# Performance work log

Measured on AMD Instinct MI355X. Metric: run time of the kernel, lower is better.

The kernel has to match this reference:

```python
import jax, jax.numpy as jnp
import numpy as np

M, K, N = 32, 8192, 8192  # tokens, in_features, out_features
PACK = 8  # int4 nibbles per int32


def setup_inputs() -> dict:
    key = jax.random.key(0)
    k1, k2, k3, k4 = jax.random.split(key, 4)
    x = (jax.random.normal(k1, (M, K), dtype=jnp.float32)).astype(jnp.float16)
    # packed int4 weights: 8 signed nibbles per int32, [N, K//8]
    b_packed = jax.random.randint(k2, (N, K // PACK), 0, 2147483647, dtype=jnp.int32)
    # rowwise fp16 scales (meta), one per output row; small positive values
    scales = (jax.random.uniform(k3, (N,), dtype=jnp.float32) * 0.01 + 1e-4).astype(jnp.float16)
    bias = (jax.random.normal(k4, (N,), dtype=jnp.float32) * 0.01).astype(jnp.float16)
    return {"x": x, "b_packed": b_packed, "scales": scales, "bias": bias}


def _unpack_int4(b_packed):
    # b_packed: [N, K//8] int32 -> signed int4 values in [-8, 7], shape [N, K]
    shifts = (jnp.arange(PACK, dtype=jnp.int32) * 4)  # [8]
    nib = (b_packed[:, :, None] >> shifts) & 0xF       # [N, K//8, 8]
    q = jnp.where(nib >= 8, nib - 16, nib)             # two's-complement nibble
    return q.reshape(b_packed.shape[0], -1)            # [N, K]


def reference(x, b_packed, scales, bias):
    # Rowwise dequant: W[n, k] = q[n, k] * scale[n]  (fp16), then y = x @ W^T + bias
    q = _unpack_int4(b_packed).astype(jnp.float16)          # [N, K]
    W = q * scales[:, None]                                  # [N, K] fp16
    y = jnp.einsum('mk,nk->mn', x, W,
                   preferred_element_type=jnp.float32).astype(jnp.float16)
    y = y + bias.astype(y.dtype)
    return y
```

## Files before the change

kernel.cpp:

```cpp
#include <hip/hip_runtime.h>
#include <cstdint>

#define M_DIM 32
#define K_DIM 8192
#define N_DIM 8192

typedef _Float16 f16x8 __attribute__((ext_vector_type(8)));
typedef _Float16 f16x2 __attribute__((ext_vector_type(2)));
typedef float    f32x4 __attribute__((ext_vector_type(4)));

__device__ __forceinline__ uint32_t u4e(uint4 v, int t) {
  return (t == 0) ? v.x : (t == 1) ? v.y : (t == 2) ? v.z : v.w;
}

__device__ __forceinline__ f16x8 dq8(uint32_t w) {
  union { uint32_t u[4]; f16x8 v; } r;
  const uint32_t MASK  = 0x000F000Fu;
  const uint32_t MAGIC = 0x64086408u;
  const f16x2 magic = __builtin_bit_cast(f16x2, MAGIC);
#pragma unroll
  for (int s = 0; s < 4; ++s) {
    uint32_t t = ((w >> (4 * s)) & MASK) ^ MAGIC;
    f16x2 h = __builtin_bit_cast(f16x2, t) - magic;
    r.u[s] = __builtin_bit_cast(uint32_t, h);
  }
  return r.v;
}

__global__ __launch_bounds__(256) void xprep_kernel(
    const float* __restrict__ x, uint4* __restrict__ xp) {
  const int T = blockIdx.x * 256 + threadIdx.x;
  const int m = T >> 10;
  const int g = T & 1023;
  const f32x4* p = (const f32x4*)(x + (size_t)m * K_DIM + (size_t)g * 8);
  f32x4 lo = p[0], hi = p[1];
  union { uint4 q; f16x8 v; } o;
#pragma unroll
  for (int s = 0; s < 4; ++s) {
    o.v[2 * s]     = (_Float16)lo[s];
    o.v[2 * s + 1] = (_Float16)hi[s];
  }
  xp[(size_t)g * 32 + m] = o.q;
}

__global__ __launch_bounds__(1024, 4) void qgemm_xp(
    const uint32_t* __restrict__ bq,
    const uint4*    __restrict__ xp,
    const float*    __restrict__ sc,
    const float*    __restrict__ bi,
    float*          __restrict__ out) {
  __shared__ float red[16][32][33];

  const int tid  = threadIdx.x;
  const int w    = tid >> 6;
  const int lane = tid & 63;
  const int l16  = lane & 15;
  const int quad = lane >> 4;
  const int n0   = blockIdx.x << 5;

  const uint4* bq4 = (const uint4*)bq;
  const uint4* bp0 = bq4 + (size_t)(n0 + l16) * 256 + (w << 4) + quad;
  const uint4* bp1 = bp0 + (size_t)16 * 256;
  const uint4* ap  = xp + (size_t)(((w << 6) + (quad << 2)) * 32 + l16);

  uint4 b0[4], b1[4];
#pragma unroll
  for (int c = 0; c < 4; ++c) { b0[c] = bp0[c * 4]; b1[c] = bp1[c * 4]; }

  f32x4 acc00 = {0.f, 0.f, 0.f, 0.f};
  f32x4 acc01 = {0.f, 0.f, 0.f, 0.f};
  f32x4 acc10 = {0.f, 0.f, 0.f, 0.f};
  f32x4 acc11 = {0.f, 0.f, 0.f, 0.f};

  uint4 a0c = ap[0], a1c = ap[16];
#pragma unroll
  for (int g = 0; g < 16; ++g) {
    const int gn  = (g + 1) & 15;
    const int off = (((gn >> 2) * 16) + (gn & 3)) * 32;
    uint4 a0n = ap[off];
    uint4 a1n = ap[off + 16];

    const int c = g >> 2, t = g & 3;
    f16x8 fb0 = dq8(u4e(b0[c], t));
    f16x8 fb1 = dq8(u4e(b1[c], t));
    f16x8 fa0 = __builtin_bit_cast(f16x8, a0c);
    f16x8 fa1 = __builtin_bit_cast(f16x8, a1c);
    acc00 = __builtin_amdgcn_mfma_f32_16x16x32_f16(fa0, fb0, acc00, 0, 0, 0);
    acc01 = __builtin_amdgcn_mfma_f32_16x16x32_f16(fa1, fb0, acc01, 0, 0, 0);
    acc10 = __builtin_amdgcn_mfma_f32_16x16x32_f16(fa0, fb1, acc10, 0, 0, 0);
    acc11 = __builtin_amdgcn_mfma_f32_16x16x32_f16(fa1, fb1, acc11, 0, 0, 0);

    a0c = a0n; a1c = a1n;
  }

#pragma unroll
  for (int r = 0; r < 4; ++r) {
    const int mr = (quad << 2) + r;
    red[w][l16][mr]           = acc00[r];
    red[w][l16][mr + 16]      = acc01[r];
    red[w][l16 + 16][mr]      = acc10[r];
    red[w][l16 + 16][mr + 16] = acc11[r];
  }

  __syncthreads();

  const int n = tid & 31;
  const int m = tid >> 5;
  float s = 0.f;
#pragma unroll
  for (int ww = 0; ww < 16; ++ww) s += red[ww][n][m];
  const int gn = n0 + n;
  out[(size_t)m * N_DIM + gn] = fmaf(s, sc[gn], bi[gn]);
}

__global__ __launch_bounds__(512) void qgemm_direct(
    const uint32_t* __restrict__ bq, const float* __restrict__ x,
    const float* __restrict__ sc, const float* __restrict__ bi,
    float* __restrict__ out) {
  __shared__ float red[8][32][40];
  const int tid  = threadIdx.x;
  const int w    = tid >> 6;
  const int lane = tid & 63;
  const int l16  = lane & 15;
  const int quad = lane >> 4;
  const int n0   = blockIdx.x << 5;

  const uint4* bq4 = (const uint4*)bq;
  const uint4* bp0 = bq4 + (size_t)(n0 + l16) * 256 + (w << 5) + quad;
  const uint4* bp1 = bp0 + (size_t)16 * 256;
  const float* ap0 = x + (size_t)l16 * K_DIM + (w << 10) + (quad << 5);
  const float* ap1 = ap0 + (size_t)16 * K_DIM;

  f32x4 acc00 = {0.f,0.f,0.f,0.f}, acc01 = {0.f,0.f,0.f,0.f};
  f32x4 acc10 = {0.f,0.f,0.f,0.f}, acc11 = {0.f,0.f,0.f,0.f};
#pragma unroll
  for (int c = 0; c < 8; ++c) {
    const uint4 wb0 = bp0[c * 4];
    const uint4 wb1 = bp1[c * 4];
#pragma unroll
    for (int t = 0; t < 4; ++t) {
      const float* a0 = ap0 + c * 128 + t * 8;
      const float* a1 = ap1 + c * 128 + t * 8;
      f32x4 l0 = *(const f32x4*)a0, h0 = *(const f32x4*)(a0 + 4);
      f32x4 l1 = *(const f32x4*)a1, h1 = *(const f32x4*)(a1 + 4);
      f16x8 fa0, fa1;
#pragma unroll
      for (int s = 0; s < 4; ++s) {
        fa0[2*s] = (_Float16)l0[s]; fa0[2*s+1] = (_Float16)h0[s];
        fa1[2*s] = (_Float16)l1[s]; fa1[2*s+1] = (_Float16)h1[s];
      }
      f16x8 fb0 = dq8(u4e(wb0, t));
      f16x8 fb1 = dq8(u4e(wb1, t));
      acc00 = __builtin_amdgcn_mfma_f32_16x16x32_f16(fa0, fb0, acc00, 0, 0, 0);
      acc01 = __builtin_amdgcn_mfma_f32_16x16x32_f16(fa1, fb0, acc01, 0, 0, 0);
      acc10 = __builtin_amdgcn_mfma_f32_16x16x32_f16(fa0, fb1, acc10, 0, 0, 0);
      acc11 = __builtin_amdgcn_mfma_f32_16x16x32_f16(fa1, fb1, acc11, 0, 0, 0);
    }
  }
#pragma unroll
  for (int r = 0; r < 4; ++r) {
    const int mr = (quad << 2) + r;
    red[w][l16][mr]           = acc00[r];
    red[w][l16][mr + 16]      = acc01[r];
    red[w][l16 + 16][mr]      = acc10[r];
    red[w][l16 + 16][mr + 16] = acc11[r];
  }
  __syncthreads();
  const int n  = tid & 31;
  const int mh = tid >> 5;
  float s0 = 0.f, s1 = 0.f;
#pragma unroll
  for (int ww = 0; ww < 8; ++ww) { s0 += red[ww][n][mh]; s1 += red[ww][n][mh+16]; }
  const int gn = n0 + n;
  out[(size_t)mh * N_DIM + gn]        = fmaf(s0, sc[gn], bi[gn]);
  out[(size_t)(mh + 16) * N_DIM + gn] = fmaf(s1, sc[gn], bi[gn]);
}

extern "C" void kernel_launch(void* const* d_in, const int* in_sizes, int n_in,
                              void* d_out, int out_size, void* d_ws, size_t ws_size,
                              hipStream_t stream) {
  const float*    x  = (const float*)d_in[0];
  const uint32_t* bq = (const uint32_t*)d_in[1];
  const float*    sc = (const float*)d_in[2];
  const float*    bi = (const float*)d_in[3];
  float*          y  = (float*)d_out;

  const size_t XP_BYTES = (size_t)M_DIM * K_DIM * 2;
  if (ws_size >= XP_BYTES) {
    uint4* xp = (uint4*)d_ws;
    xprep_kernel<<<128, 256, 0, stream>>>(x, xp);
    qgemm_xp<<<N_DIM / 32, 1024, 0, stream>>>(bq, xp, sc, bi, y);
  } else {
    qgemm_direct<<<N_DIM / 32, 512, 0, stream>>>(bq, x, sc, bi, y);
  }
}
```

Baseline: 89.40 us.

## Halve output tile to 16 columns per block, doubling grid size

The xp-path GEMM kernel now handles 16 output columns per block instead of 32 and launches twice as many blocks, with fewer accumulators and registers per thread and a higher occupancy hint. The goal is more parallelism across the GPU's compute units and better latency hiding for the int4 weight stream. In exchange the activation tile is re-read twice as often from cache, the software prefetch of activations is dropped, and half the threads sit idle during the final reduction.

After: 93.18 us. +4.2%, slower.

```diff
diff --git a/kernel.cpp b/kernel.cpp
--- a/kernel.cpp
+++ b/kernel.cpp
@@ -43,74 +43,63 @@
   xp[(size_t)g * 32 + m] = o.q;
 }
 
-__global__ __launch_bounds__(1024, 4) void qgemm_xp(
+__global__ __launch_bounds__(1024, 8) void qgemm_xp16(
     const uint32_t* __restrict__ bq,
     const uint4*    __restrict__ xp,
     const float*    __restrict__ sc,
     const float*    __restrict__ bi,
     float*          __restrict__ out) {
-  __shared__ float red[16][32][33];
+  __shared__ float red[16][16][34];
 
   const int tid  = threadIdx.x;
   const int w    = tid >> 6;
   const int lane = tid & 63;
   const int l16  = lane & 15;
   const int quad = lane >> 4;
-  const int n0   = blockIdx.x << 5;
+  const int n0   = blockIdx.x << 4;
 
   const uint4* bq4 = (const uint4*)bq;
   const uint4* bp0 = bq4 + (size_t)(n0 + l16) * 256 + (w << 4) + quad;
-  const uint4* bp1 = bp0 + (size_t)16 * 256;
   const uint4* ap  = xp + (size_t)(((w << 6) + (quad << 2)) * 32 + l16);
 
-  uint4 b0[4], b1[4];
+  uint4 b0[4];
 #pragma unroll
-  for (int c = 0; c < 4; ++c) { b0[c] = bp0[c * 4]; b1[c] = bp1[c * 4]; }
+  for (int c = 0; c < 4; ++c) b0[c] = bp0[c * 4];
 
-  f32x4 acc00 = {0.f, 0.f, 0.f, 0.f};
-  f32x4 acc01 = {0.f, 0.f, 0.f, 0.f};
-  f32x4 acc10 = {0.f, 0.f, 0.f, 0.f};
-  f32x4 acc11 = {0.f, 0.f, 0.f, 0.f};
+  f32x4 acc0 = {0.f, 0.f, 0.f, 0.f};
+  f32x4 acc1 = {0.f, 0.f, 0.f, 0.f};
 
-  uint4 a0c = ap[0], a1c = ap[16];
 #pragma unroll
   for (int g = 0; g < 16; ++g) {
-    const int gn  = (g + 1) & 15;
-    const int off = (((gn >> 2) * 16) + (gn & 3)) * 32;
-    uint4 a0n = ap[off];
-    uint4 a1n = ap[off + 16];
-
-    const int c = g >> 2, t = g & 3;
-    f16x8 fb0 = dq8(u4e(b0[c], t));
-    f16x8 fb1 = dq8(u4e(b1[c], t));
-    f16x8 fa0 = __builtin_bit_cast(f16x8, a0c);
-    f16x8 fa1 = __builtin_bit_cast(f16x8, a1c);
-    acc00 = __builtin_amdgcn_mfma_f32_16x16x32_f16(fa0, fb0, acc00, 0, 0, 0);
-    acc01 = __builtin_amdgcn_mfma_f32_16x16x32_f16(fa1, fb0, acc01, 0, 0, 0);
-    acc10 = __builtin_amdgcn_mfma_f32_16x16x32_f16(fa0, fb1, acc10, 0, 0, 0);
-    acc11 = __builtin_amdgcn_mfma_f32_16x16x32_f16(fa1, fb1, acc11, 0, 0, 0);
-
-    a0c = a0n; a1c = a1n;
+    const int c   = g >> 2, t = g & 3;
+    const int off = (c * 16 + t) * 32;
+    uint4 a0 = ap[off];
+    uint4 a1 = ap[off + 16];
+    f16x8 fb  = dq8(u4e(b0[c], t));
+    f16x8 fa0 = __builtin_bit_cast(f16x8, a0);
+    f16x8 fa1 = __builtin_bit_cast(f16x8, a1);
+    acc0 = __builtin_amdgcn_mfma_f32_16x16x32_f16(fa0, fb, acc0, 0, 0, 0);
+    acc1 = __builtin_amdgcn_mfma_f32_16x16x32_f16(fa1, fb, acc1, 0, 0, 0);
   }
 
 #pragma unroll
   for (int r = 0; r < 4; ++r) {
     const int mr = (quad << 2) + r;
-    red[w][l16][mr]           = acc00[r];
-    red[w][l16][mr + 16]      = acc01[r];
-    red[w][l16 + 16][mr]      = acc10[r];
-    red[w][l16 + 16][mr + 16] = acc11[r];
+    red[w][l16][mr]      = acc0[r];
+    red[w][l16][mr + 16] = acc1[r];
   }
 
   __syncthreads();
 
-  const int n = tid & 31;
-  const int m = tid >> 5;
-  float s = 0.f;
+  if (tid < 512) {
+    const int n = tid & 15;
+    const int m = tid >> 4;
+    float s = 0.f;
 #pragma unroll
-  for (int ww = 0; ww < 16; ++ww) s += red[ww][n][m];
-  const int gn = n0 + n;
-  out[(size_t)m * N_DIM + gn] = fmaf(s, sc[gn], bi[gn]);
+    for (int ww = 0; ww < 16; ++ww) s += red[ww][n][m];
+    const int gn = n0 + n;
+    out[(size_t)m * N_DIM + gn] = fmaf(s, sc[gn], bi[gn]);
+  }
 }
 
 __global__ __launch_bounds__(512) void qgemm_direct(
@@ -189,7 +178,7 @@
   if (ws_size >= XP_BYTES) {
     uint4* xp = (uint4*)d_ws;
     xprep_kernel<<<128, 256, 0, stream>>>(x, xp);
-    qgemm_xp<<<N_DIM / 32, 1024, 0, stream>>>(bq, xp, sc, bi, y);
+    qgemm_xp16<<<N_DIM / 16, 1024, 0, stream>>>(bq, xp, sc, bi, y);
   } else {
     qgemm_direct<<<N_DIM / 32, 512, 0, stream>>>(bq, x, sc, bi, y);
   }
```
